# Kernel optimization log

Hardware: AMD Instinct MI355X
Metric: run time of the kernel (lower is better)

Reference implementation:

```python
import jax, jax.numpy as jnp
import numpy as np

N_NODES = 100000
FEAT_DIM = 256
EMBED_DIM = 256
BATCH = 50000
NUM_SAMPLE = 10


def setup_inputs() -> dict:
    key = jax.random.key(0)
    k1, k2, k3, k4 = jax.random.split(key, 4)
    features = jax.random.normal(k1, (N_NODES, FEAT_DIM), dtype=jnp.float32)
    # weight: [embed_dim, 2*feat_dim] (gcn=False path), xavier-like scale
    weight = jax.random.normal(k2, (EMBED_DIM, 2 * FEAT_DIM), dtype=jnp.float32)
    weight = weight * jnp.sqrt(2.0 / (EMBED_DIM + 2 * FEAT_DIM))
    nodes = jax.random.randint(k3, (BATCH,), 0, N_NODES, dtype=jnp.int64)
    neigh_idx = jax.random.randint(k4, (BATCH, NUM_SAMPLE), 0, N_NODES, dtype=jnp.int64)
    return {"features": features, "weight": weight, "nodes": nodes, "neigh_idx": neigh_idx}


def reference(features, weight, nodes, neigh_idx):
    # MeanAggregator: gather sampled neighbor feats and average over samples
    neigh_feats = features[neigh_idx].mean(axis=1)          # [B, F]
    self_feats = features[nodes]                             # [B, F]
    combined = jnp.concatenate([self_feats, neigh_feats], axis=1)  # [B, 2F]
    # weight.mm(combined.t()) -> [embed_dim, B], then relu
    out = jax.nn.relu(weight @ combined.T)
    return out
```

## Files before the change

### kernel.cpp

```cpp
#include <hip/hip_runtime.h>

#define FEAT   256
#define K2     512
#define NNODES 100000
#define BATCH  50000
#define NS     10
#define EMBED  256
#define BN     32
#define NBLK   ((BATCH + BN - 1) / BN)

typedef __attribute__((ext_vector_type(8))) __bf16         bf16x8;
typedef __attribute__((ext_vector_type(8))) unsigned short ushort8;
typedef __attribute__((ext_vector_type(4))) float          f32x4;
typedef __attribute__((ext_vector_type(2))) float          f32x2;
typedef __attribute__((ext_vector_type(2))) int            i32x2;
typedef __attribute__((ext_vector_type(4))) int            i32x4;

static __device__ __forceinline__ unsigned short f2bf(float x) {
    unsigned int u = __builtin_bit_cast(unsigned int, x);
    u += 0x7FFFu + ((u >> 16) & 1u);
    return (unsigned short)(u >> 16);
}
static __device__ __forceinline__ float bf2f(unsigned short h) {
    return __builtin_bit_cast(float, (unsigned int)h << 16);
}
static __device__ __forceinline__ void gload16(void* lds, const void* g) {
    __builtin_amdgcn_global_load_lds(
        (const __attribute__((address_space(1))) void*)g,
        (__attribute__((address_space(3))) void*)lds, 16, 0, 0);
}

__global__ void fconv_kernel(const float* __restrict__ f,
                             unsigned short* __restrict__ fb,
                             unsigned char* __restrict__ f8) {
    int i = blockIdx.x * blockDim.x + threadIdx.x;
    const f32x4* src = (const f32x4*)(f + (size_t)i * 8);
    f32x4 a = __builtin_nontemporal_load(src);
    f32x4 b = __builtin_nontemporal_load(src + 1);
    ushort8 h;
    h[0]=f2bf(a[0]); h[1]=f2bf(a[1]); h[2]=f2bf(a[2]); h[3]=f2bf(a[3]);
    h[4]=f2bf(b[0]); h[5]=f2bf(b[1]); h[6]=f2bf(b[2]); h[7]=f2bf(b[3]);
    ((ushort8*)fb)[i] = h;
    int u0 = 0, u1 = 0;
    u0 = __builtin_amdgcn_cvt_pk_fp8_f32(a[0], a[1], u0, false);
    u0 = __builtin_amdgcn_cvt_pk_fp8_f32(a[2], a[3], u0, true);
    u1 = __builtin_amdgcn_cvt_pk_fp8_f32(b[0], b[1], u1, false);
    u1 = __builtin_amdgcn_cvt_pk_fp8_f32(b[2], b[3], u1, true);
    i32x2 p; p[0] = u0; p[1] = u1;
    ((i32x2*)f8)[i] = p;
}

__global__ void wpack_kernel(const float* __restrict__ w,
                             unsigned short* __restrict__ wp) {
    int c    = blockIdx.x * blockDim.x + threadIdx.x;
    int lane = c & 63;
    int ks   = (c >> 6) & 1;
    int mblk = (c >> 7) & 15;
    int kt   = c >> 11;
    int row  = mblk * 16 + (lane & 15);
    int col  = kt * 64 + ks * 32 + (lane >> 4) * 8;
    const f32x4* src = (const f32x4*)(w + row * K2 + col);
    f32x4 a = src[0], b = src[1];
    ushort8 h;
    h[0]=f2bf(a[0]); h[1]=f2bf(a[1]); h[2]=f2bf(a[2]); h[3]=f2bf(a[3]);
    h[4]=f2bf(b[0]); h[5]=f2bf(b[1]); h[6]=f2bf(b[2]); h[7]=f2bf(b[3]);
    ((ushort8*)wp)[c] = h;
}

__global__ __launch_bounds__(512, 4) void gemm_dma(
    const unsigned short* __restrict__ fbf,
    const unsigned char* __restrict__ ffp8,
    const unsigned short* __restrict__ wp,
    const int* __restrict__ nodes,
    const int* __restrict__ neigh,
    float* __restrict__ out) {

    __shared__ __align__(16) unsigned short lB[BN * K2];
    __shared__ __align__(16) unsigned char  s8[3][BN * FEAT];

    const int tid  = threadIdx.x;
    const int nb0  = blockIdx.x * BN;
    const int w    = tid >> 6;
    const int lane = tid & 63;
    const char* fbb = (const char*)fbf;
    const char* f8b = (const char*)ffp8;

    int off_s[4];
    #pragma unroll
    for (int j = 0; j < 4; ++j)
        off_s[j] = nodes[min(nb0 + 4 * w + j, BATCH - 1)] << 9;
    const int nrow = min(nb0 + 4 * w + (lane >> 4), BATCH - 1);
    int on[NS];
    #pragma unroll
    for (int s = 0; s < NS; ++s)
        on[s] = neigh[nrow * NS + s] << 8;
    asm volatile("s_waitcnt vmcnt(0)" ::: "memory");

    #pragma unroll
    for (int j = 0; j < 4; ++j) {
        const int r = 4 * w + j, rx = r & 7;
        if (lane < 32) {
            const int c  = lane;
            const int cs = (c & ~7) | ((c & 7) ^ rx);
            gload16(&lB[r * K2], fbb + off_s[j] + cs * 16);
        }
    }
    #pragma unroll
    for (int s = 0; s < 3; ++s)
        gload16(&s8[s][w * 1024], f8b + on[s] + (lane & 15) * 16);

    const int cr  = tid >> 4;
    const int ch  = tid & 15;
    const int crx = cr & 7;
    float acc[16];
    #pragma unroll
    for (int e = 0; e < 16; ++e) acc[e] = 0.f;

    #pragma unroll
    for (int s = 0; s < NS; ++s) {
        if (s <= 7)      asm volatile("s_waitcnt vmcnt(2)" ::: "memory");
        else if (s == 8) asm volatile("s_waitcnt vmcnt(1)" ::: "memory");
        else             asm volatile("s_waitcnt vmcnt(0)" ::: "memory");
        __builtin_amdgcn_s_barrier();
        __builtin_amdgcn_sched_barrier(0);

        i32x4 v = *(const i32x4*)&s8[s % 3][cr * 256 + ch * 16];
        #pragma unroll
        for (int q = 0; q < 4; ++q) {
            f32x2 lo = __builtin_amdgcn_cvt_pk_f32_fp8(v[q], false);
            f32x2 hi = __builtin_amdgcn_cvt_pk_f32_fp8(v[q], true);
            acc[q * 4 + 0] += lo[0];
            acc[q * 4 + 1] += lo[1];
            acc[q * 4 + 2] += hi[0];
            acc[q * 4 + 3] += hi[1];
        }
        __builtin_amdgcn_sched_barrier(0);
        __builtin_amdgcn_s_barrier();
        __builtin_amdgcn_sched_barrier(0);
        if (s + 3 < NS)
            gload16(&s8[s % 3][w * 1024], f8b + on[s + 3] + (lane & 15) * 16);
    }

    {
        ushort8 a, b;
        #pragma unroll
        for (int e = 0; e < 8; ++e) {
            a[e] = f2bf(acc[e] * 0.1f);
            b[e] = f2bf(acc[8 + e] * 0.1f);
        }
        const int g = 4 + (ch >> 2), i0 = (ch & 3) * 2;
        unsigned short* dst = lB + cr * K2 + g * 64;
        *(ushort8*)&dst[((i0    ) ^ crx) * 8] = a;
        *(ushort8*)&dst[((i0 + 1) ^ crx) * 8] = b;
    }
    __syncthreads();

    const int lr = lane & 15;
    const int lg = lane >> 4;

    f32x4 facc[2][2] = {};

    #pragma unroll
    for (int kt = 0; kt < 8; ++kt) {
        bf16x8 af[2][2], bfr[2][2];
        #pragma unroll
        for (int i = 0; i < 2; ++i)
            #pragma unroll
            for (int ks = 0; ks < 2; ++ks)
                af[i][ks] = *(const bf16x8*)(wp +
                    ((((kt * 16 + w * 2 + i) * 2 + ks) * 64 + lane) << 3));
        #pragma unroll
        for (int j = 0; j < 2; ++j) {
            const int rb = j * 16 + lr;
            #pragma unroll
            for (int ks = 0; ks < 2; ++ks) {
                int cc = kt * 8 + ((ks * 4 + lg) ^ (rb & 7));
                bfr[j][ks] = *(const bf16x8*)&lB[rb * K2 + cc * 8];
            }
        }
        #pragma unroll
        for (int ks = 0; ks < 2; ++ks)
            #pragma unroll
            for (int i = 0; i < 2; ++i)
                #pragma unroll
                for (int j = 0; j < 2; ++j)
                    facc[i][j] = __builtin_amdgcn_mfma_f32_16x16x32_bf16(
                        af[i][ks], bfr[j][ks], facc[i][j], 0, 0, 0);
    }

    #pragma unroll
    for (int j = 0; j < 2; ++j) {
        const int n2 = nb0 + j * 16 + lr;
        if (n2 < BATCH) {
            #pragma unroll
            for (int i = 0; i < 2; ++i) {
                int m0 = w * 32 + i * 16 + lg * 4;
                #pragma unroll
                for (int rg = 0; rg < 4; ++rg) {
                    float v = facc[i][j][rg];
                    v = v > 0.f ? v : 0.f;
                    __builtin_nontemporal_store(v, &out[(size_t)(m0 + rg) * BATCH + n2]);
                }
            }
        }
    }
}

__global__ __launch_bounds__(512, 4) void gemm_f32(
    const float* __restrict__ features,
    const unsigned short* __restrict__ wp,
    const int* __restrict__ nodes,
    const int* __restrict__ neigh,
    float* __restrict__ out) {

    __shared__ __align__(16) unsigned short lB[BN * K2];

    const int tid = threadIdx.x;
    const int nb0 = blockIdx.x * BN;
    const int r  = tid >> 4;
    const int h  = tid & 15;
    const int rx = r & 7;
    const int n  = nb0 + r;
    const bool valid = n < BATCH;

    int node0 = valid ? nodes[n] : 0;
    int nidx[NS];
    #pragma unroll
    for (int s = 0; s < NS; ++s) nidx[s] = valid ? neigh[n * NS + s] : 0;

    ushort8 a = {0,0,0,0,0,0,0,0}, b = a;
    if (valid) {
        const f32x4* s0 = (const f32x4*)(features + (size_t)node0 * FEAT + h * 16);
        f32x4 x0 = s0[0], x1 = s0[1], x2 = s0[2], x3 = s0[3];
        a[0]=f2bf(x0[0]); a[1]=f2bf(x0[1]); a[2]=f2bf(x0[2]); a[3]=f2bf(x0[3]);
        a[4]=f2bf(x1[0]); a[5]=f2bf(x1[1]); a[6]=f2bf(x1[2]); a[7]=f2bf(x1[3]);
        b[0]=f2bf(x2[0]); b[1]=f2bf(x2[1]); b[2]=f2bf(x2[2]); b[3]=f2bf(x2[3]);
        b[4]=f2bf(x3[0]); b[5]=f2bf(x3[1]); b[6]=f2bf(x3[2]); b[7]=f2bf(x3[3]);
    }
    {
        const int g = h >> 2, i0 = (h & 3) * 2;
        unsigned short* dst = lB + r * K2 + g * 64;
        *(ushort8*)&dst[((i0    ) ^ rx) * 8] = a;
        *(ushort8*)&dst[((i0 + 1) ^ rx) * 8] = b;
    }
    {
        float acc[16];
        #pragma unroll
        for (int e = 0; e < 16; ++e) acc[e] = 0.f;
        #pragma unroll
        for (int s = 0; s < NS; ++s) {
            const f32x4* p = (const f32x4*)(features + (size_t)nidx[s] * FEAT + h * 16);
            f32x4 x0 = p[0], x1 = p[1], x2 = p[2], x3 = p[3];
            #pragma unroll
            for (int e = 0; e < 4; ++e) {
                acc[e]      += x0[e];
                acc[4 + e]  += x1[e];
                acc[8 + e]  += x2[e];
                acc[12 + e] += x3[e];
            }
        }
        ushort8 aa, bb;
        #pragma unroll
        for (int e = 0; e < 8; ++e) {
            aa[e] = f2bf(valid ? acc[e]     * 0.1f : 0.f);
            bb[e] = f2bf(valid ? acc[8 + e] * 0.1f : 0.f);
        }
        const int g = 4 + (h >> 2), i0 = (h & 3) * 2;
        unsigned short* dst = lB + r * K2 + g * 64;
        *(ushort8*)&dst[((i0    ) ^ rx) * 8] = aa;
        *(ushort8*)&dst[((i0 + 1) ^ rx) * 8] = bb;
    }
    __syncthreads();

    const int w    = tid >> 6;
    const int lane = tid & 63;
    const int lr   = lane & 15;
    const int lg   = lane >> 4;

    f32x4 facc[2][2] = {};
    #pragma unroll
    for (int kt = 0; kt < 8; ++kt) {
        bf16x8 af[2][2], bfr[2][2];
        #pragma unroll
        for (int i = 0; i < 2; ++i)
            #pragma unroll
            for (int ks = 0; ks < 2; ++ks)
                af[i][ks] = *(const bf16x8*)(wp +
                    ((((kt * 16 + w * 2 + i) * 2 + ks) * 64 + lane) << 3));
        #pragma unroll
        for (int j = 0; j < 2; ++j) {
            const int rb = j * 16 + lr;
            #pragma unroll
            for (int ks = 0; ks < 2; ++ks) {
                int cc = kt * 8 + ((ks * 4 + lg) ^ (rb & 7));
                bfr[j][ks] = *(const bf16x8*)&lB[rb * K2 + cc * 8];
            }
        }
        #pragma unroll
        for (int ks = 0; ks < 2; ++ks)
            #pragma unroll
            for (int i = 0; i < 2; ++i)
                #pragma unroll
                for (int j = 0; j < 2; ++j)
                    facc[i][j] = __builtin_amdgcn_mfma_f32_16x16x32_bf16(
                        af[i][ks], bfr[j][ks], facc[i][j], 0, 0, 0);
    }
    #pragma unroll
    for (int j = 0; j < 2; ++j) {
        const int n2 = nb0 + j * 16 + lr;
        if (n2 < BATCH) {
            #pragma unroll
            for (int i = 0; i < 2; ++i) {
                int m0 = w * 32 + i * 16 + lg * 4;
                #pragma unroll
                for (int rg = 0; rg < 4; ++rg) {
                    float v = facc[i][j][rg];
                    v = v > 0.f ? v : 0.f;
                    __builtin_nontemporal_store(v, &out[(size_t)(m0 + rg) * BATCH + n2]);
                }
            }
        }
    }
}

extern "C" void kernel_launch(void* const* d_in, const int* in_sizes, int n_in,
                              void* d_out, int out_size, void* d_ws, size_t ws_size,
                              hipStream_t stream) {
    const float* features = (const float*)d_in[0];
    const float* weight   = (const float*)d_in[1];
    const int*   nodes    = (const int*)d_in[2];
    const int*   neigh    = (const int*)d_in[3];
    float* out = (float*)d_out;

    unsigned short* wp   = (unsigned short*)d_ws;
    unsigned short* fbf  = wp + (size_t)EMBED * K2;
    unsigned char*  ffp8 = (unsigned char*)(fbf + (size_t)NNODES * FEAT);

    const size_t need = (size_t)EMBED * K2 * 2 + (size_t)NNODES * FEAT * 3;

    wpack_kernel<<<(EMBED * K2 / 8) / 256, 256, 0, stream>>>(weight, wp);

    if (ws_size >= need) {
        fconv_kernel<<<(NNODES * FEAT / 8) / 256, 256, 0, stream>>>(features, fbf, ffp8);
        gemm_dma<<<NBLK, 512, 0, stream>>>(fbf, ffp8, wp, nodes, neigh, out);
    } else {
        gemm_f32<<<NBLK, 512, 0, stream>>>(features, wp, nodes, neigh, out);
    }
}
```

Before: 85.47 us.

## Split neighbor mean into sharded XCD-local gather kernel before GEMM

The fp8 feature table is stored as 8 column shards of 32 bytes per node, so each shard is a 3.2MB table. A new nmean_kernel assigns blockIdx&7 to a shard, which appears aimed at keeping each shard resident in one XCD's L2 while gathering and averaging the 10 neighbors. The averages are written to a bf16 workspace that a simplified GEMM kernel reads directly. This removes the in-GEMM fp8 gather pipeline and its barriers, at the cost of an extra launch, an extra intermediate write/read of 50000x256 bf16, and a larger workspace requirement.

```diff
diff --git a/kernel.cpp b/kernel.cpp
--- a/kernel.cpp
+++ b/kernel.cpp
@@ -8,6 +8,8 @@
 #define EMBED  256
 #define BN     32
 #define NBLK   ((BATCH + BN - 1) / BN)
+#define NSH    8
+#define SHC    32
 
 typedef __attribute__((ext_vector_type(8))) __bf16         bf16x8;
 typedef __attribute__((ext_vector_type(8))) unsigned short ushort8;
@@ -30,6 +32,7 @@
         (__attribute__((address_space(3))) void*)lds, 16, 0, 0);
 }
 
+template <bool SHARD>
 __global__ void fconv_kernel(const float* __restrict__ f,
                              unsigned short* __restrict__ fb,
                              unsigned char* __restrict__ f8) {
@@ -47,7 +50,13 @@
     u1 = __builtin_amdgcn_cvt_pk_fp8_f32(b[0], b[1], u1, false);
     u1 = __builtin_amdgcn_cvt_pk_fp8_f32(b[2], b[3], u1, true);
     i32x2 p; p[0] = u0; p[1] = u1;
-    ((i32x2*)f8)[i] = p;
+    if (SHARD) {
+        int node = i >> 5, c8 = i & 31;
+        int shard = c8 >> 2, off = (c8 & 3) * 8;
+        *(i32x2*)(f8 + ((size_t)shard * NNODES + node) * SHC + off) = p;
+    } else {
+        ((i32x2*)f8)[i] = p;
+    }
 }
 
 __global__ void wpack_kernel(const float* __restrict__ w,
@@ -67,6 +76,140 @@
     ((ushort8*)wp)[c] = h;
 }
 
+__global__ __launch_bounds__(256, 8) void nmean_kernel(
+    const unsigned char* __restrict__ f8s,
+    const int* __restrict__ neigh,
+    unsigned short* __restrict__ nm) {
+    const int shard = blockIdx.x & 7;
+    const int n     = (blockIdx.x >> 3) * 64 + (threadIdx.x >> 2);
+    const int piece = threadIdx.x & 3;
+    if (n >= BATCH) return;
+    const unsigned char* tab = f8s + (size_t)shard * NNODES * SHC + piece * 8;
+
+    int idx[NS];
+    #pragma unroll
+    for (int s = 0; s < NS; ++s)
+        idx[s] = __builtin_nontemporal_load(&neigh[n * NS + s]);
+
+    float acc[8];
+    #pragma unroll
+    for (int e = 0; e < 8; ++e) acc[e] = 0.f;
+    #pragma unroll
+    for (int s = 0; s < NS; ++s) {
+        i32x2 v = *(const i32x2*)(tab + (size_t)idx[s] * SHC);
+        #pragma unroll
+        for (int q = 0; q < 2; ++q) {
+            f32x2 lo = __builtin_amdgcn_cvt_pk_f32_fp8(v[q], false);
+            f32x2 hi = __builtin_amdgcn_cvt_pk_f32_fp8(v[q], true);
+            acc[q * 4 + 0] += lo[0];
+            acc[q * 4 + 1] += lo[1];
+            acc[q * 4 + 2] += hi[0];
+            acc[q * 4 + 3] += hi[1];
+        }
+    }
+    ushort8 o;
+    #pragma unroll
+    for (int e = 0; e < 8; ++e) o[e] = f2bf(acc[e] * 0.1f);
+    __builtin_nontemporal_store(o,
+        (ushort8*)(nm + ((size_t)shard * BATCH + n) * SHC + piece * 8));
+}
+
+__global__ __launch_bounds__(512, 4) void gemm_xcd(
+    const unsigned short* __restrict__ fbf,
+    const unsigned short* __restrict__ nm_,
+    const unsigned short* __restrict__ wp,
+    const int* __restrict__ nodes,
+    float* __restrict__ out) {
+
+    __shared__ __align__(16) unsigned short lB[BN * K2];
+
+    const int tid  = threadIdx.x;
+    const int nb0  = blockIdx.x * BN;
+    const int w    = tid >> 6;
+    const int lane = tid & 63;
+    const char* fbb = (const char*)fbf;
+
+    const int r_nm = lane >> 1;
+    const int n_nm = min(nb0 + r_nm, BATCH - 1);
+    const ushort8* nmp = (const ushort8*)(nm_ +
+        ((size_t)w * BATCH + n_nm) * SHC + (lane & 1) * 16);
+    ushort8 d0 = nmp[0], d1 = nmp[1];
+
+    int off_s[4];
+    #pragma unroll
+    for (int j = 0; j < 4; ++j)
+        off_s[j] = nodes[min(nb0 + 4 * w + j, BATCH - 1)] << 9;
+    #pragma unroll
+    for (int j = 0; j < 4; ++j) {
+        const int r = 4 * w + j, rx = r & 7;
+        if (lane < 32) {
+            const int cs = (lane & ~7) | ((lane & 7) ^ rx);
+            gload16(&lB[r * K2], fbb + off_s[j] + cs * 16);
+        }
+    }
+    __builtin_amdgcn_sched_barrier(0);
+
+    {
+        const int rx = r_nm & 7;
+        const int g  = 4 + (w >> 1);
+        const int i0 = (w & 1) * 4 + (lane & 1) * 2;
+        unsigned short* dst = lB + r_nm * K2 + g * 64;
+        *(ushort8*)&dst[((i0    ) ^ rx) * 8] = d0;
+        *(ushort8*)&dst[((i0 + 1) ^ rx) * 8] = d1;
+    }
+    asm volatile("s_waitcnt vmcnt(0)" ::: "memory");
+    __syncthreads();
+
+    const int lr = lane & 15;
+    const int lg = lane >> 4;
+    f32x4 facc[2][2] = {};
+
+    #pragma unroll
+    for (int kt = 0; kt < 8; ++kt) {
+        bf16x8 af[2][2], bfr[2][2];
+        #pragma unroll
+        for (int i = 0; i < 2; ++i)
+            #pragma unroll
+            for (int ks = 0; ks < 2; ++ks)
+                af[i][ks] = *(const bf16x8*)(wp +
+                    ((((kt * 16 + w * 2 + i) * 2 + ks) * 64 + lane) << 3));
+        #pragma unroll
+        for (int j = 0; j < 2; ++j) {
+            const int rb = j * 16 + lr;
+            #pragma unroll
+            for (int ks = 0; ks < 2; ++ks) {
+                int cc = kt * 8 + ((ks * 4 + lg) ^ (rb & 7));
+                bfr[j][ks] = *(const bf16x8*)&lB[rb * K2 + cc * 8];
+            }
+        }
+        #pragma unroll
+        for (int ks = 0; ks < 2; ++ks)
+            #pragma unroll
+            for (int i = 0; i < 2; ++i)
+                #pragma unroll
+                for (int j = 0; j < 2; ++j)
+                    facc[i][j] = __builtin_amdgcn_mfma_f32_16x16x32_bf16(
+                        af[i][ks], bfr[j][ks], facc[i][j], 0, 0, 0);
+    }
+
+    #pragma unroll
+    for (int j = 0; j < 2; ++j) {
+        const int n2 = nb0 + j * 16 + lr;
+        if (n2 < BATCH) {
+            #pragma unroll
+            for (int i = 0; i < 2; ++i) {
+                int m0 = w * 32 + i * 16 + lg * 4;
+                #pragma unroll
+                for (int rg = 0; rg < 4; ++rg) {
+                    float v = facc[i][j][rg];
+                    v = v > 0.f ? v : 0.f;
+                    __builtin_nontemporal_store(v, &out[(size_t)(m0 + rg) * BATCH + n2]);
+                }
+            }
+        }
+    }
+}
+
 __global__ __launch_bounds__(512, 4) void gemm_dma(
     const unsigned short* __restrict__ fbf,
     const unsigned char* __restrict__ ffp8,
@@ -100,8 +243,7 @@
     for (int j = 0; j < 4; ++j) {
         const int r = 4 * w + j, rx = r & 7;
         if (lane < 32) {
-            const int c  = lane;
-            const int cs = (c & ~7) | ((c & 7) ^ rx);
+            const int cs = (lane & ~7) | ((lane & 7) ^ rx);
             gload16(&lB[r * K2], fbb + off_s[j] + cs * 16);
         }
     }
@@ -140,7 +282,6 @@
         if (s + 3 < NS)
             gload16(&s8[s % 3][w * 1024], f8b + on[s + 3] + (lane & 15) * 16);
     }
-
     {
         ushort8 a, b;
         #pragma unroll
@@ -157,9 +298,7 @@
 
     const int lr = lane & 15;
     const int lg = lane >> 4;
-
     f32x4 facc[2][2] = {};
-
     #pragma unroll
     for (int kt = 0; kt < 8; ++kt) {
         bf16x8 af[2][2], bfr[2][2];
@@ -187,7 +326,6 @@
                     facc[i][j] = __builtin_amdgcn_mfma_f32_16x16x32_bf16(
                         af[i][ks], bfr[j][ks], facc[i][j], 0, 0, 0);
     }
-
     #pragma unroll
     for (int j = 0; j < 2; ++j) {
         const int n2 = nb0 + j * 16 + lr;
@@ -334,15 +472,21 @@
 
     unsigned short* wp   = (unsigned short*)d_ws;
     unsigned short* fbf  = wp + (size_t)EMBED * K2;
-    unsigned char*  ffp8 = (unsigned char*)(fbf + (size_t)NNODES * FEAT);
-
-    const size_t need = (size_t)EMBED * K2 * 2 + (size_t)NNODES * FEAT * 3;
+    unsigned char*  f8   = (unsigned char*)(fbf + (size_t)NNODES * FEAT);
+    unsigned short* nm   = (unsigned short*)(f8 + (size_t)NNODES * FEAT);
+
+    const size_t need_t2   = (size_t)EMBED * K2 * 2 + (size_t)NNODES * FEAT * 3;
+    const size_t need_full = need_t2 + (size_t)NSH * BATCH * SHC * 2;
 
     wpack_kernel<<<(EMBED * K2 / 8) / 256, 256, 0, stream>>>(weight, wp);
 
-    if (ws_size >= need) {
-        fconv_kernel<<<(NNODES * FEAT / 8) / 256, 256, 0, stream>>>(features, fbf, ffp8);
-        gemm_dma<<<NBLK, 512, 0, stream>>>(fbf, ffp8, wp, nodes, neigh, out);
+    if (ws_size >= need_full) {
+        fconv_kernel<true><<<(NNODES * FEAT / 8) / 256, 256, 0, stream>>>(features, fbf, f8);
+        nmean_kernel<<<NSH * ((BATCH + 63) / 64), 256, 0, stream>>>(f8, neigh, nm);
+        gemm_xcd<<<NBLK, 512, 0, stream>>>(fbf, nm, wp, nodes, out);
+    } else if (ws_size >= need_t2) {
+        fconv_kernel<false><<<(NNODES * FEAT / 8) / 256, 256, 0, stream>>>(features, fbf, f8);
+        gemm_dma<<<NBLK, 512, 0, stream>>>(fbf, f8, wp, nodes, neigh, out);
     } else {
         gemm_f32<<<NBLK, 512, 0, stream>>>(features, wp, nodes, neigh, out);
     }
```

Measured after the change: 110.4 us. +29.1%, slower.

## Drop bf16 feature table; gather self rows from fp32 and neighbors from fp8

Applied to the files above, without the earlier changes.

The conversion kernel now writes only an fp8 copy of the feature table instead of both bf16 and fp8, which cuts its write traffic. The main kernel drops the LDS-DMA triple-buffered pipeline. Self rows are read directly from fp32 features and converted to bf16 in registers, and neighbor rows are read from the fp8 table with plain vector loads. This trades the explicit async prefetch and barriers for simpler code that relies on the hardware to hide latency, and the self rows are now read at fp32 width.

```diff
diff --git a/kernel.cpp b/kernel.cpp
--- a/kernel.cpp
+++ b/kernel.cpp
@@ -21,26 +21,12 @@
     u += 0x7FFFu + ((u >> 16) & 1u);
     return (unsigned short)(u >> 16);
 }
-static __device__ __forceinline__ float bf2f(unsigned short h) {
-    return __builtin_bit_cast(float, (unsigned int)h << 16);
-}
-static __device__ __forceinline__ void gload16(void* lds, const void* g) {
-    __builtin_amdgcn_global_load_lds(
-        (const __attribute__((address_space(1))) void*)g,
-        (__attribute__((address_space(3))) void*)lds, 16, 0, 0);
-}
 
 __global__ void fconv_kernel(const float* __restrict__ f,
-                             unsigned short* __restrict__ fb,
                              unsigned char* __restrict__ f8) {
     int i = blockIdx.x * blockDim.x + threadIdx.x;
     const f32x4* src = (const f32x4*)(f + (size_t)i * 8);
-    f32x4 a = __builtin_nontemporal_load(src);
-    f32x4 b = __builtin_nontemporal_load(src + 1);
-    ushort8 h;
-    h[0]=f2bf(a[0]); h[1]=f2bf(a[1]); h[2]=f2bf(a[2]); h[3]=f2bf(a[3]);
-    h[4]=f2bf(b[0]); h[5]=f2bf(b[1]); h[6]=f2bf(b[2]); h[7]=f2bf(b[3]);
-    ((ushort8*)fb)[i] = h;
+    f32x4 a = src[0], b = src[1];
     int u0 = 0, u1 = 0;
     u0 = __builtin_amdgcn_cvt_pk_fp8_f32(a[0], a[1], u0, false);
     u0 = __builtin_amdgcn_cvt_pk_fp8_f32(a[2], a[3], u0, true);
@@ -67,96 +53,77 @@
     ((ushort8*)wp)[c] = h;
 }
 
-__global__ __launch_bounds__(512, 4) void gemm_dma(
-    const unsigned short* __restrict__ fbf,
-    const unsigned char* __restrict__ ffp8,
+__global__ __launch_bounds__(512, 4) void gemm_hyb(
+    const float* __restrict__ features,
+    const unsigned char* __restrict__ f8,
     const unsigned short* __restrict__ wp,
     const int* __restrict__ nodes,
     const int* __restrict__ neigh,
     float* __restrict__ out) {
 
     __shared__ __align__(16) unsigned short lB[BN * K2];
-    __shared__ __align__(16) unsigned char  s8[3][BN * FEAT];
-
-    const int tid  = threadIdx.x;
-    const int nb0  = blockIdx.x * BN;
+
+    const int tid = threadIdx.x;
+    const int nb0 = blockIdx.x * BN;
+    const int r   = tid >> 4;
+    const int p   = tid & 15;
+    const int rx  = r & 7;
+    const int n   = min(nb0 + r, BATCH - 1);
+
+    {
+        const int node0 = nodes[n];
+        const f32x4* s0 = (const f32x4*)(features + (size_t)node0 * FEAT + p * 16);
+        f32x4 x0 = s0[0], x1 = s0[1], x2 = s0[2], x3 = s0[3];
+        ushort8 a, b;
+        a[0]=f2bf(x0[0]); a[1]=f2bf(x0[1]); a[2]=f2bf(x0[2]); a[3]=f2bf(x0[3]);
+        a[4]=f2bf(x1[0]); a[5]=f2bf(x1[1]); a[6]=f2bf(x1[2]); a[7]=f2bf(x1[3]);
+        b[0]=f2bf(x2[0]); b[1]=f2bf(x2[1]); b[2]=f2bf(x2[2]); b[3]=f2bf(x2[3]);
+        b[4]=f2bf(x3[0]); b[5]=f2bf(x3[1]); b[6]=f2bf(x3[2]); b[7]=f2bf(x3[3]);
+        const int g = p >> 2, i0 = (p & 3) * 2;
+        unsigned short* dst = lB + r * K2 + g * 64;
+        *(ushort8*)&dst[((i0    ) ^ rx) * 8] = a;
+        *(ushort8*)&dst[((i0 + 1) ^ rx) * 8] = b;
+    }
+
+    {
+        int idx[NS];
+        #pragma unroll
+        for (int s = 0; s < NS; ++s) idx[s] = neigh[n * NS + s];
+
+        float acc[16];
+        #pragma unroll
+        for (int e = 0; e < 16; ++e) acc[e] = 0.f;
+
+        #pragma unroll
+        for (int s = 0; s < NS; ++s) {
+            i32x4 v = *(const i32x4*)(f8 + (size_t)idx[s] * FEAT + p * 16);
+            #pragma unroll
+            for (int q = 0; q < 4; ++q) {
+                f32x2 lo = __builtin_amdgcn_cvt_pk_f32_fp8(v[q], false);
+                f32x2 hi = __builtin_amdgcn_cvt_pk_f32_fp8(v[q], true);
+                acc[q * 4 + 0] += lo[0];
+                acc[q * 4 + 1] += lo[1];
+                acc[q * 4 + 2] += hi[0];
+                acc[q * 4 + 3] += hi[1];
+            }
+        }
+        ushort8 a, b;
+        #pragma unroll
+        for (int e = 0; e < 8; ++e) {
+            a[e] = f2bf(acc[e]     * 0.1f);
+            b[e] = f2bf(acc[8 + e] * 0.1f);
+        }
+        const int g = 4 + (p >> 2), i0 = (p & 3) * 2;
+        unsigned short* dst = lB + r * K2 + g * 64;
+        *(ushort8*)&dst[((i0    ) ^ rx) * 8] = a;
+        *(ushort8*)&dst[((i0 + 1) ^ rx) * 8] = b;
+    }
+    __syncthreads();
+
     const int w    = tid >> 6;
     const int lane = tid & 63;
-    const char* fbb = (const char*)fbf;
-    const char* f8b = (const char*)ffp8;
-
-    int off_s[4];
-    #pragma unroll
-    for (int j = 0; j < 4; ++j)
-        off_s[j] = nodes[min(nb0 + 4 * w + j, BATCH - 1)] << 9;
-    const int nrow = min(nb0 + 4 * w + (lane >> 4), BATCH - 1);
-    int on[NS];
-    #pragma unroll
-    for (int s = 0; s < NS; ++s)
-        on[s] = neigh[nrow * NS + s] << 8;
-    asm volatile("s_waitcnt vmcnt(0)" ::: "memory");
-
-    #pragma unroll
-    for (int j = 0; j < 4; ++j) {
-        const int r = 4 * w + j, rx = r & 7;
-        if (lane < 32) {
-            const int c  = lane;
-            const int cs = (c & ~7) | ((c & 7) ^ rx);
-            gload16(&lB[r * K2], fbb + off_s[j] + cs * 16);
-        }
-    }
-    #pragma unroll
-    for (int s = 0; s < 3; ++s)
-        gload16(&s8[s][w * 1024], f8b + on[s] + (lane & 15) * 16);
-
-    const int cr  = tid >> 4;
-    const int ch  = tid & 15;
-    const int crx = cr & 7;
-    float acc[16];
-    #pragma unroll
-    for (int e = 0; e < 16; ++e) acc[e] = 0.f;
-
-    #pragma unroll
-    for (int s = 0; s < NS; ++s) {
-        if (s <= 7)      asm volatile("s_waitcnt vmcnt(2)" ::: "memory");
-        else if (s == 8) asm volatile("s_waitcnt vmcnt(1)" ::: "memory");
-        else             asm volatile("s_waitcnt vmcnt(0)" ::: "memory");
-        __builtin_amdgcn_s_barrier();
-        __builtin_amdgcn_sched_barrier(0);
-
-        i32x4 v = *(const i32x4*)&s8[s % 3][cr * 256 + ch * 16];
-        #pragma unroll
-        for (int q = 0; q < 4; ++q) {
-            f32x2 lo = __builtin_amdgcn_cvt_pk_f32_fp8(v[q], false);
-            f32x2 hi = __builtin_amdgcn_cvt_pk_f32_fp8(v[q], true);
-            acc[q * 4 + 0] += lo[0];
-            acc[q * 4 + 1] += lo[1];
-            acc[q * 4 + 2] += hi[0];
-            acc[q * 4 + 3] += hi[1];
-        }
-        __builtin_amdgcn_sched_barrier(0);
-        __builtin_amdgcn_s_barrier();
-        __builtin_amdgcn_sched_barrier(0);
-        if (s + 3 < NS)
-            gload16(&s8[s % 3][w * 1024], f8b + on[s + 3] + (lane & 15) * 16);
-    }
-
-    {
-        ushort8 a, b;
-        #pragma unroll
-        for (int e = 0; e < 8; ++e) {
-            a[e] = f2bf(acc[e] * 0.1f);
-            b[e] = f2bf(acc[8 + e] * 0.1f);
-        }
-        const int g = 4 + (ch >> 2), i0 = (ch & 3) * 2;
-        unsigned short* dst = lB + cr * K2 + g * 64;
-        *(ushort8*)&dst[((i0    ) ^ crx) * 8] = a;
-        *(ushort8*)&dst[((i0 + 1) ^ crx) * 8] = b;
-    }
-    __syncthreads();
-
-    const int lr = lane & 15;
-    const int lg = lane >> 4;
+    const int lr   = lane & 15;
+    const int lg   = lane >> 4;
 
     f32x4 facc[2][2] = {};
 
@@ -220,24 +187,21 @@
     const int r  = tid >> 4;
     const int h  = tid & 15;
     const int rx = r & 7;
-    const int n  = nb0 + r;
-    const bool valid = n < BATCH;
-
-    int node0 = valid ? nodes[n] : 0;
+    const int n  = min(nb0 + r, BATCH - 1);
+
+    int node0 = nodes[n];
     int nidx[NS];
     #pragma unroll
-    for (int s = 0; s < NS; ++s) nidx[s] = valid ? neigh[n * NS + s] : 0;
-
-    ushort8 a = {0,0,0,0,0,0,0,0}, b = a;
-    if (valid) {
+    for (int s = 0; s < NS; ++s) nidx[s] = neigh[n * NS + s];
+
+    {
         const f32x4* s0 = (const f32x4*)(features + (size_t)node0 * FEAT + h * 16);
         f32x4 x0 = s0[0], x1 = s0[1], x2 = s0[2], x3 = s0[3];
+        ushort8 a, b;
         a[0]=f2bf(x0[0]); a[1]=f2bf(x0[1]); a[2]=f2bf(x0[2]); a[3]=f2bf(x0[3]);
         a[4]=f2bf(x1[0]); a[5]=f2bf(x1[1]); a[6]=f2bf(x1[2]); a[7]=f2bf(x1[3]);
         b[0]=f2bf(x2[0]); b[1]=f2bf(x2[1]); b[2]=f2bf(x2[2]); b[3]=f2bf(x2[3]);
         b[4]=f2bf(x3[0]); b[5]=f2bf(x3[1]); b[6]=f2bf(x3[2]); b[7]=f2bf(x3[3]);
-    }
-    {
         const int g = h >> 2, i0 = (h & 3) * 2;
         unsigned short* dst = lB + r * K2 + g * 64;
         *(ushort8*)&dst[((i0    ) ^ rx) * 8] = a;
@@ -249,8 +213,8 @@
         for (int e = 0; e < 16; ++e) acc[e] = 0.f;
         #pragma unroll
         for (int s = 0; s < NS; ++s) {
-            const f32x4* p = (const f32x4*)(features + (size_t)nidx[s] * FEAT + h * 16);
-            f32x4 x0 = p[0], x1 = p[1], x2 = p[2], x3 = p[3];
+            const f32x4* pp = (const f32x4*)(features + (size_t)nidx[s] * FEAT + h * 16);
+            f32x4 x0 = pp[0], x1 = pp[1], x2 = pp[2], x3 = pp[3];
             #pragma unroll
             for (int e = 0; e < 4; ++e) {
                 acc[e]      += x0[e];
@@ -262,8 +226,8 @@
         ushort8 aa, bb;
         #pragma unroll
         for (int e = 0; e < 8; ++e) {
-            aa[e] = f2bf(valid ? acc[e]     * 0.1f : 0.f);
-            bb[e] = f2bf(valid ? acc[8 + e] * 0.1f : 0.f);
+            aa[e] = f2bf(acc[e]     * 0.1f);
+            bb[e] = f2bf(acc[8 + e] * 0.1f);
         }
         const int g = 4 + (h >> 2), i0 = (h & 3) * 2;
         unsigned short* dst = lB + r * K2 + g * 64;
@@ -332,17 +296,16 @@
     const int*   neigh    = (const int*)d_in[3];
     float* out = (float*)d_out;
 
-    unsigned short* wp   = (unsigned short*)d_ws;
-    unsigned short* fbf  = wp + (size_t)EMBED * K2;
-    unsigned char*  ffp8 = (unsigned char*)(fbf + (size_t)NNODES * FEAT);
-
-    const size_t need = (size_t)EMBED * K2 * 2 + (size_t)NNODES * FEAT * 3;
+    unsigned short* wp = (unsigned short*)d_ws;
+    unsigned char*  f8 = (unsigned char*)(wp + (size_t)EMBED * K2);
+
+    const size_t need = (size_t)EMBED * K2 * 2 + (size_t)NNODES * FEAT;
 
     wpack_kernel<<<(EMBED * K2 / 8) / 256, 256, 0, stream>>>(weight, wp);
 
     if (ws_size >= need) {
-        fconv_kernel<<<(NNODES * FEAT / 8) / 256, 256, 0, stream>>>(features, fbf, ffp8);
-        gemm_dma<<<NBLK, 512, 0, stream>>>(fbf, ffp8, wp, nodes, neigh, out);
+        fconv_kernel<<<(NNODES * FEAT / 8) / 256, 256, 0, stream>>>(features, f8);
+        gemm_hyb<<<NBLK, 512, 0, stream>>>(features, f8, wp, nodes, neigh, out);
     } else {
         gemm_f32<<<NBLK, 512, 0, stream>>>(features, wp, nodes, neigh, out);
     }
```

Measured after the change: 74.20 us. 1.15x faster.
